# Kernel optimization log

Hardware: AMD Instinct MI355X
Metric: run time of the kernel (lower is better)

The kernel has to match this reference:

```python
import jax, jax.numpy as jnp
import numpy as np

NEG_BIG = -1.0e9


def setup_inputs() -> dict:
    key = jax.random.key(0)
    kq, kk, kv, km = jax.random.split(key, 4)
    B, H, S, D = 8, 16, 1024, 64
    q = jax.random.normal(kq, (B, H, S, D), dtype=jnp.float32)
    k = jax.random.normal(kk, (B, H, S, D), dtype=jnp.float32)
    v = jax.random.normal(kv, (B, H, S, D), dtype=jnp.float32)
    mask = jax.random.uniform(km, (S - 1, S - 1), dtype=jnp.float32)
    return {"q": q, "k": k, "v": v, "mask": mask}


def reference(q, k, v, mask):
    # scores: [B,H,S,S]
    dk = k.shape[-1]
    logits = jnp.einsum("bhsd,bhtd->bhst", q, k) / jnp.sqrt(jnp.asarray(dk, q.dtype))
    if mask is not None:
        # original adds mask*-1e9 only on logits[:, :, 1:, 1:];
        # equivalent to padding mask with a zero first row/col then adding.
        mask_padded = jnp.pad(mask, ((1, 0), (1, 0)))  # [S, S]
        logits = logits + mask_padded * NEG_BIG
    attention_weights = jax.nn.softmax(logits, axis=-1)
    output = jnp.einsum("bhst,bhtd->bhsd", attention_weights, v)
    return (output, attention_weights)
```

## Files before the change

kernel.cpp:

```cpp
#include <hip/hip_runtime.h>

#define S_LEN 1024
#define D_DIM 64
#define QB 16
#define NTHREADS 1024
#define LSTR 1036
#define ESTR 2072
#define ELO 1024
#define RINV_OFF 66304
#define LDS_BYTES 66368

typedef short s16x8 __attribute__((ext_vector_type(8)));
typedef short s16x4 __attribute__((ext_vector_type(4)));
typedef float f32x4 __attribute__((ext_vector_type(4)));
typedef unsigned short u16;
typedef unsigned int u32;

static __device__ __forceinline__ u16 f2bf_rne(float f) {
  u32 u = __builtin_bit_cast(u32, f);
  return (u16)((u + 0x7fffu + ((u >> 16) & 1u)) >> 16);
}

static __device__ __forceinline__ void split2(float f, u16& h, u16& l) {
  u32 u = __builtin_bit_cast(u32, f);
  h = (u16)(u >> 16);
  float hf = __builtin_bit_cast(float, u & 0xffff0000u);
  l = f2bf_rne(f - hf);
}

static __device__ __forceinline__ f32x4 mfma16(s16x8 a, s16x8 b, f32x4 c) {
  return __builtin_amdgcn_mfma_f32_16x16x32_bf16(a, b, c, 0, 0, 0);
}

static __device__ __forceinline__ void cvt8(f32x4 a, f32x4 b, s16x8& h, s16x8& l) {
  s16x8 hh, ll;
#pragma unroll
  for (int j = 0; j < 8; ++j) {
    float fj = (j < 4) ? a[j] : b[j - 4];
    u16 hb, lb;
    split2(fj, hb, lb);
    hh[j] = (short)hb;
    ll[j] = (short)lb;
  }
  h = hh; l = ll;
}

extern "C" __global__ void __launch_bounds__(NTHREADS, 8)
attn_fused(const float* __restrict__ qg, const float* __restrict__ kg,
           const float* __restrict__ vg, const float* __restrict__ mg,
           float* __restrict__ og, float* __restrict__ wg)
{
  extern __shared__ char smem[];
  float* L = (float*)smem;
  u16* E = (u16*)smem;
  float* sc = (float*)smem;
  float* rinv = (float*)(smem + RINV_OFF);

  const int tid = threadIdx.x;
  const int wave = tid >> 6;
  const int lane = tid & 63;
  const int l15 = lane & 15;
  const int lg4 = lane >> 4;

  const int bid = (int)blockIdx.x;
  const int swz = (bid & 7) * 1024 + (bid >> 3);
  const int qb = swz & 63;
  const int bh = swz >> 6;
  const int qbase = qb * QB;

  const float* qp = qg + (size_t)bh * S_LEN * D_DIM;
  const float* kp = kg + (size_t)bh * S_LEN * D_DIM;
  const float* vp = vg + (size_t)bh * S_LEN * D_DIM;

  {
    s16x8 qh[2], ql[2];
    const float* qrow = qp + (size_t)(qbase + l15) * D_DIM + lg4 * 8;
#pragma unroll
    for (int ks = 0; ks < 2; ++ks) {
      f32x4 a = *(const f32x4*)(qrow + ks * 32);
      f32x4 b = *(const f32x4*)(qrow + ks * 32 + 4);
#pragma unroll
      for (int j = 0; j < 4; ++j) { a[j] *= 0.125f; b[j] *= 0.125f; }
      cvt8(a, b, qh[ks], ql[ks]);
    }

#pragma unroll 1
    for (int ct = 0; ct < 4; ++ct) {
      const int t = wave * 64 + ct * 16 + l15;
      const float* krow = kp + (size_t)t * D_DIM + lg4 * 8;
      s16x8 kh[2], kl[2];
#pragma unroll
      for (int ks = 0; ks < 2; ++ks) {
        f32x4 a = *(const f32x4*)(krow + ks * 32);
        f32x4 b = *(const f32x4*)(krow + ks * 32 + 4);
        cvt8(a, b, kh[ks], kl[ks]);
      }
      f32x4 acc = {0.f, 0.f, 0.f, 0.f};
#pragma unroll
      for (int ks = 0; ks < 2; ++ks) {
        acc = mfma16(qh[ks], kh[ks], acc);
        acc = mfma16(qh[ks], kl[ks], acc);
        acc = mfma16(ql[ks], kh[ks], acc);
      }
#pragma unroll
      for (int j = 0; j < 4; ++j) {
        const int rl = lg4 * 4 + j;
        const int s = qbase + rl;
        float mv = 0.f;
        if (s > 0 && t > 0) mv = mg[(size_t)(s - 1) * (S_LEN - 1) + (t - 1)];
        L[rl * LSTR + t] = fmaf(mv, -1.0e9f, acc[j]);
      }
    }
  }
  __syncthreads();

  {
    const float* Lr = L + wave * LSTR;
    float m = -3.402823466e38f;
#pragma unroll
    for (int g = 0; g < 4; ++g) {
      f32x4 lv = *(const f32x4*)&Lr[lane * 4 + g * 256];
#pragma unroll
      for (int j = 0; j < 4; ++j) m = fmaxf(m, lv[j]);
    }
#pragma unroll
    for (int off = 1; off < 64; off <<= 1) m = fmaxf(m, __shfl_xor(m, off, 64));

    f32x4 e[4];
    float sum = 0.f;
#pragma unroll
    for (int g = 0; g < 4; ++g) {
      f32x4 lv = *(const f32x4*)&Lr[lane * 4 + g * 256];
#pragma unroll
      for (int j = 0; j < 4; ++j) {
        float ex = __expf(lv[j] - m);
        e[g][j] = ex;
        sum += ex;
      }
    }
#pragma unroll
    for (int off = 1; off < 64; off <<= 1) sum += __shfl_xor(sum, off, 64);
    const float inv = 1.0f / sum;
    if (lane == 0) rinv[wave] = inv;

    float* wrow = wg + (size_t)bh * S_LEN * S_LEN + (size_t)(qbase + wave) * S_LEN;
    u16* Er = E + wave * ESTR;
#pragma unroll
    for (int g = 0; g < 4; ++g) {
      const int col = lane * 4 + g * 256;
      f32x4 wv;
      s16x4 eh, el;
#pragma unroll
      for (int j = 0; j < 4; ++j) {
        wv[j] = e[g][j] * inv;
        u16 hb, lb;
        split2(e[g][j], hb, lb);
        eh[j] = (short)hb;
        el[j] = (short)lb;
      }
      *(f32x4*)&wrow[col] = wv;
      *(s16x4*)&Er[col] = eh;
      *(s16x4*)&Er[ELO + col] = el;
    }
  }
  __syncthreads();

  const int g3 = wave >> 2;
  const int ct = wave & 3;
  const int dcol = ct * 16 + l15;
  f32x4 acc = {0.f, 0.f, 0.f, 0.f};
#pragma unroll 2
  for (int T = g3 * 8; T < g3 * 8 + 8; ++T) {
    const int t0 = T * 32 + lg4 * 8;
    s16x8 vh, vl;
#pragma unroll
    for (int i = 0; i < 8; ++i) {
      u16 hb, lb;
      split2(vp[(size_t)(t0 + i) * D_DIM + dcol], hb, lb);
      vh[i] = (short)hb;
      vl[i] = (short)lb;
    }
    s16x8 ah = *(const s16x8*)&E[l15 * ESTR + t0];
    s16x8 al = *(const s16x8*)&E[l15 * ESTR + ELO + t0];
    acc = mfma16(ah, vh, acc);
    acc = mfma16(ah, vl, acc);
    acc = mfma16(al, vh, acc);
  }
  __syncthreads();

#pragma unroll
  for (int j = 0; j < 4; ++j)
    sc[g3 * 1024 + (lg4 * 4 + j) * 64 + dcol] = acc[j];
  __syncthreads();

  {
    const int q = wave;
    const int d = lane;
    float s = sc[q * 64 + d] + sc[1024 + q * 64 + d] +
              sc[2048 + q * 64 + d] + sc[3072 + q * 64 + d];
    og[(size_t)bh * S_LEN * D_DIM + (size_t)(qbase + q) * D_DIM + d] = s * rinv[q];
  }
}

extern "C" void kernel_launch(void* const* d_in, const int* in_sizes, int n_in,
                              void* d_out, int out_size, void* d_ws, size_t ws_size,
                              hipStream_t stream) {
  const float* q = (const float*)d_in[0];
  const float* k = (const float*)d_in[1];
  const float* v = (const float*)d_in[2];
  const float* m = (const float*)d_in[3];
  float* out = (float*)d_out;
  float* w = out + (size_t)8 * 16 * S_LEN * D_DIM;

  hipFuncSetAttribute((const void*)attn_fused,
                      hipFuncAttributeMaxDynamicSharedMemorySize, LDS_BYTES);
  attn_fused<<<dim3(8192), NTHREADS, LDS_BYTES, stream>>>(q, k, v, m, out, w);
}
```

Measured before the change: 1.018 ms.

## Pre-split K and transposed V into bf16 hi/lo workspace before attention

Adds two pre-pass kernels. One splits K into bf16 hi/lo halves. The other splits V and transposes it, writing both into the workspace. The main kernel then loads ready-made bf16 vectors instead of redoing the fp32-to-bf16 split in each of the 64 query blocks per head, and V becomes contiguous 16-byte loads instead of strided scalar gathers. It also makes the weight and output stores nontemporal and keeps the logits in registers during softmax. The cost is two extra launches, a workspace requirement, and extra traffic writing and reading the split copies. The old path is kept as a fallback when the workspace is too small.

```diff
diff --git a/kernel.cpp b/kernel.cpp
--- a/kernel.cpp
+++ b/kernel.cpp
@@ -10,6 +10,10 @@
 #define RINV_OFF 66304
 #define LDS_BYTES 66368
 
+#define NBH 128
+#define KV_ELEMS ((size_t)NBH * S_LEN * D_DIM)
+#define WS_NEED (KV_ELEMS * 8)
+
 typedef short s16x8 __attribute__((ext_vector_type(8)));
 typedef short s16x4 __attribute__((ext_vector_type(4)));
 typedef float f32x4 __attribute__((ext_vector_type(4)));
@@ -45,10 +49,54 @@
   h = hh; l = ll;
 }
 
-extern "C" __global__ void __launch_bounds__(NTHREADS, 8)
+extern "C" __global__ void __launch_bounds__(256)
+presplit_k(const float* __restrict__ kg, u16* __restrict__ khi, u16* __restrict__ klo) {
+  const size_t base = ((size_t)blockIdx.x * 256 + threadIdx.x) * 8;
+  f32x4 a = __builtin_nontemporal_load((const f32x4*)(kg + base));
+  f32x4 b = __builtin_nontemporal_load((const f32x4*)(kg + base + 4));
+  s16x8 h, l;
+  cvt8(a, b, h, l);
+  *(s16x8*)(khi + base) = h;
+  *(s16x8*)(klo + base) = l;
+}
+
+extern "C" __global__ void __launch_bounds__(256)
+presplit_vt(const float* __restrict__ vg, u16* __restrict__ vthi, u16* __restrict__ vtlo) {
+  __shared__ u16 ht[64][72];
+  __shared__ u16 lt[64][72];
+  const int tid = threadIdx.x;
+  const int bh = blockIdx.x >> 4;
+  const int t0 = (blockIdx.x & 15) * 64;
+  const float* vp = vg + ((size_t)bh * S_LEN + t0) * D_DIM;
+#pragma unroll
+  for (int it = 0; it < 16; ++it) {
+    const int idx = it * 256 + tid;
+    float f = __builtin_nontemporal_load(vp + idx);
+    u16 h, l;
+    split2(f, h, l);
+    ht[idx & 63][idx >> 6] = h;
+    lt[idx & 63][idx >> 6] = l;
+  }
+  __syncthreads();
+#pragma unroll
+  for (int o = tid; o < 2048; o += 256) {
+    const int d = o >> 5;
+    const int tp = (o & 31) * 2;
+    u32 wh = (u32)ht[d][tp] | ((u32)ht[d][tp + 1] << 16);
+    u32 wl = (u32)lt[d][tp] | ((u32)lt[d][tp + 1] << 16);
+    const size_t off = ((size_t)bh * D_DIM + d) * S_LEN + t0 + tp;
+    *(u32*)(vthi + off) = wh;
+    *(u32*)(vtlo + off) = wl;
+  }
+}
+
+template <bool PRE>
+__global__ __launch_bounds__(NTHREADS, 8) void
 attn_fused(const float* __restrict__ qg, const float* __restrict__ kg,
            const float* __restrict__ vg, const float* __restrict__ mg,
-           float* __restrict__ og, float* __restrict__ wg)
+           float* __restrict__ og, float* __restrict__ wg,
+           const u16* __restrict__ khi, const u16* __restrict__ klo,
+           const u16* __restrict__ vthi, const u16* __restrict__ vtlo)
 {
   extern __shared__ char smem[];
   float* L = (float*)smem;
@@ -69,8 +117,6 @@
   const int qbase = qb * QB;
 
   const float* qp = qg + (size_t)bh * S_LEN * D_DIM;
-  const float* kp = kg + (size_t)bh * S_LEN * D_DIM;
-  const float* vp = vg + (size_t)bh * S_LEN * D_DIM;
 
   {
     s16x8 qh[2], ql[2];
@@ -84,16 +130,26 @@
       cvt8(a, b, qh[ks], ql[ks]);
     }
 
-#pragma unroll 1
+#pragma unroll 2
     for (int ct = 0; ct < 4; ++ct) {
       const int t = wave * 64 + ct * 16 + l15;
-      const float* krow = kp + (size_t)t * D_DIM + lg4 * 8;
       s16x8 kh[2], kl[2];
-#pragma unroll
-      for (int ks = 0; ks < 2; ++ks) {
-        f32x4 a = *(const f32x4*)(krow + ks * 32);
-        f32x4 b = *(const f32x4*)(krow + ks * 32 + 4);
-        cvt8(a, b, kh[ks], kl[ks]);
+      if constexpr (PRE) {
+        const u16* kb = khi + ((size_t)bh * S_LEN + t) * D_DIM + lg4 * 8;
+        const u16* lb = klo + ((size_t)bh * S_LEN + t) * D_DIM + lg4 * 8;
+#pragma unroll
+        for (int ks = 0; ks < 2; ++ks) {
+          kh[ks] = *(const s16x8*)(kb + ks * 32);
+          kl[ks] = *(const s16x8*)(lb + ks * 32);
+        }
+      } else {
+        const float* krow = kg + ((size_t)bh * S_LEN + t) * D_DIM + lg4 * 8;
+#pragma unroll
+        for (int ks = 0; ks < 2; ++ks) {
+          f32x4 a = *(const f32x4*)(krow + ks * 32);
+          f32x4 b = *(const f32x4*)(krow + ks * 32 + 4);
+          cvt8(a, b, kh[ks], kl[ks]);
+        }
       }
       f32x4 acc = {0.f, 0.f, 0.f, 0.f};
 #pragma unroll
@@ -116,28 +172,26 @@
 
   {
     const float* Lr = L + wave * LSTR;
+    f32x4 lv[4];
+#pragma unroll
+    for (int g = 0; g < 4; ++g) lv[g] = *(const f32x4*)&Lr[lane * 4 + g * 256];
     float m = -3.402823466e38f;
 #pragma unroll
-    for (int g = 0; g < 4; ++g) {
-      f32x4 lv = *(const f32x4*)&Lr[lane * 4 + g * 256];
-#pragma unroll
-      for (int j = 0; j < 4; ++j) m = fmaxf(m, lv[j]);
-    }
+    for (int g = 0; g < 4; ++g)
+#pragma unroll
+      for (int j = 0; j < 4; ++j) m = fmaxf(m, lv[g][j]);
 #pragma unroll
     for (int off = 1; off < 64; off <<= 1) m = fmaxf(m, __shfl_xor(m, off, 64));
 
-    f32x4 e[4];
     float sum = 0.f;
 #pragma unroll
-    for (int g = 0; g < 4; ++g) {
-      f32x4 lv = *(const f32x4*)&Lr[lane * 4 + g * 256];
+    for (int g = 0; g < 4; ++g)
 #pragma unroll
       for (int j = 0; j < 4; ++j) {
-        float ex = __expf(lv[j] - m);
-        e[g][j] = ex;
+        float ex = __expf(lv[g][j] - m);
+        lv[g][j] = ex;
         sum += ex;
       }
-    }
 #pragma unroll
     for (int off = 1; off < 64; off <<= 1) sum += __shfl_xor(sum, off, 64);
     const float inv = 1.0f / sum;
@@ -152,13 +206,13 @@
       s16x4 eh, el;
 #pragma unroll
       for (int j = 0; j < 4; ++j) {
-        wv[j] = e[g][j] * inv;
+        wv[j] = lv[g][j] * inv;
         u16 hb, lb;
-        split2(e[g][j], hb, lb);
+        split2(lv[g][j], hb, lb);
         eh[j] = (short)hb;
         el[j] = (short)lb;
       }
-      *(f32x4*)&wrow[col] = wv;
+      __builtin_nontemporal_store(wv, (f32x4*)&wrow[col]);
       *(s16x4*)&Er[col] = eh;
       *(s16x4*)&Er[ELO + col] = el;
     }
@@ -173,12 +227,18 @@
   for (int T = g3 * 8; T < g3 * 8 + 8; ++T) {
     const int t0 = T * 32 + lg4 * 8;
     s16x8 vh, vl;
-#pragma unroll
-    for (int i = 0; i < 8; ++i) {
-      u16 hb, lb;
-      split2(vp[(size_t)(t0 + i) * D_DIM + dcol], hb, lb);
-      vh[i] = (short)hb;
-      vl[i] = (short)lb;
+    if constexpr (PRE) {
+      const size_t off = ((size_t)bh * D_DIM + dcol) * S_LEN + t0;
+      vh = *(const s16x8*)(vthi + off);
+      vl = *(const s16x8*)(vtlo + off);
+    } else {
+#pragma unroll
+      for (int i = 0; i < 8; ++i) {
+        u16 hb, lb;
+        split2(vg[((size_t)bh * S_LEN + t0 + i) * D_DIM + dcol], hb, lb);
+        vh[i] = (short)hb;
+        vl[i] = (short)lb;
+      }
     }
     s16x8 ah = *(const s16x8*)&E[l15 * ESTR + t0];
     s16x8 al = *(const s16x8*)&E[l15 * ESTR + ELO + t0];
@@ -198,7 +258,8 @@
     const int d = lane;
     float s = sc[q * 64 + d] + sc[1024 + q * 64 + d] +
               sc[2048 + q * 64 + d] + sc[3072 + q * 64 + d];
-    og[(size_t)bh * S_LEN * D_DIM + (size_t)(qbase + q) * D_DIM + d] = s * rinv[q];
+    __builtin_nontemporal_store(s * rinv[q],
+        &og[(size_t)bh * S_LEN * D_DIM + (size_t)(qbase + q) * D_DIM + d]);
   }
 }
 
@@ -212,7 +273,22 @@
   float* out = (float*)d_out;
   float* w = out + (size_t)8 * 16 * S_LEN * D_DIM;
 
-  hipFuncSetAttribute((const void*)attn_fused,
-                      hipFuncAttributeMaxDynamicSharedMemorySize, LDS_BYTES);
-  attn_fused<<<dim3(8192), NTHREADS, LDS_BYTES, stream>>>(q, k, v, m, out, w);
-}
+  u16* khi = (u16*)d_ws;
+  u16* klo = khi + KV_ELEMS;
+  u16* vthi = klo + KV_ELEMS;
+  u16* vtlo = vthi + KV_ELEMS;
+
+  if (ws_size >= WS_NEED) {
+    presplit_k<<<dim3(4096), 256, 0, stream>>>(k, khi, klo);
+    presplit_vt<<<dim3(2048), 256, 0, stream>>>(v, vthi, vtlo);
+    hipFuncSetAttribute(reinterpret_cast<const void*>(attn_fused<true>),
+                        hipFuncAttributeMaxDynamicSharedMemorySize, LDS_BYTES);
+    attn_fused<true><<<dim3(8192), NTHREADS, LDS_BYTES, stream>>>(
+        q, k, v, m, out, w, khi, klo, vthi, vtlo);
+  } else {
+    hipFuncSetAttribute(reinterpret_cast<const void*>(attn_fused<false>),
+                        hipFuncAttributeMaxDynamicSharedMemorySize, LDS_BYTES);
+    attn_fused<false><<<dim3(8192), NTHREADS, LDS_BYTES, stream>>>(
+        q, k, v, m, out, w, khi, klo, vthi, vtlo);
+  }
+}
```

After: 1.092 ms. +7.3%, slower.
